# Performance work log

Measured on AMD Instinct MI355X. Metric: run time of the kernel, lower is better.

The kernel has to match this reference:

```python
import jax, jax.numpy as jnp
import numpy as np

B, S, H, D = 2, 2048, 16, 128
HID = H * D
THETA = 10000.0
SCALE = 1.0 / np.sqrt(D)


def setup_inputs() -> dict:
    key = jax.random.key(0)
    k1, k2, k3 = jax.random.split(key, 3)
    x = jax.random.normal(k1, (B, S, HID), dtype=jnp.float32)
    w_qkv = jax.random.normal(k2, (3 * HID, HID), dtype=jnp.float32) * 0.02
    w_o = jax.random.normal(k3, (HID, HID), dtype=jnp.float32) * 0.02
    return {"x": x, "w_qkv": w_qkv, "w_o": w_o}


def _rope_cos_sin(seq_len, dim, dtype):
    inv_freq = 1.0 / (THETA ** (jnp.arange(0, dim, 2, dtype=jnp.float32) / dim))
    pos = jnp.arange(seq_len, dtype=jnp.float32)
    freqs = pos[:, None] * inv_freq[None, :]          # (S, D/2)
    emb = jnp.concatenate([freqs, freqs], axis=-1)    # (S, D)
    return jnp.cos(emb).astype(dtype), jnp.sin(emb).astype(dtype)


def _rotate_half(t):
    t1, t2 = jnp.split(t, 2, axis=-1)
    return jnp.concatenate([-t2, t1], axis=-1)


def reference(x, w_qkv, w_o):
    b, s, _ = x.shape
    qkv = jnp.einsum('bsh,oh->bso', x, w_qkv)                 # (B,S,3*HID)
    qkv = qkv.reshape(b, s, 3, H, D).transpose(2, 0, 3, 1, 4)  # (3,B,H,S,D)
    q, k, v = qkv[0], qkv[1], qkv[2]
    cos, sin = _rope_cos_sin(s, D, x.dtype)                    # (S,D)
    q = q * cos + _rotate_half(q) * sin
    k = k * cos + _rotate_half(k) * sin
    scores = jnp.einsum('bhqd,bhkd->bhqk', q, k) * SCALE       # (B,H,S,S)
    causal = jnp.triu(jnp.ones((s, s), dtype=bool), k=1)
    scores = jnp.where(causal[None, None], -jnp.inf, scores)
    attn = jax.nn.softmax(scores.astype(jnp.float32), axis=-1).astype(q.dtype)
    out = jnp.einsum('bhqk,bhkd->bhqd', attn, v)               # (B,H,S,D)
    out = out.transpose(0, 2, 1, 3).reshape(b, s, HID)
    return jnp.einsum('bsh,oh->bso', out, w_o)
```

## Files before the change

### kernel.cpp

```cpp
#include <hip/hip_runtime.h>
#include <hip/hip_bf16.h>

typedef unsigned short u16;
typedef unsigned long long u64;
typedef u16 us8 __attribute__((ext_vector_type(8)));
typedef __bf16 bf8_t __attribute__((ext_vector_type(8)));
typedef float f32x4 __attribute__((ext_vector_type(4)));

__device__ __forceinline__ float b2f(u16 u) {
    return __uint_as_float(((unsigned int)u) << 16);
}
__device__ __forceinline__ u16 f2b(float f) {
    union { __hip_bfloat16 h; u16 u; } v;
    v.h = __float2bfloat16(f);
    return v.u;
}
__device__ __forceinline__ f32x4 mfma16(bf8_t a, bf8_t b, f32x4 c) {
    return __builtin_amdgcn_mfma_f32_16x16x32_bf16(a, b, c, 0, 0, 0);
}
__device__ __forceinline__ void gload_lds16(const u16* g, u16* lds_base) {
    __builtin_amdgcn_global_load_lds((const __attribute__((address_space(1))) unsigned int*)g,
                                     (__attribute__((address_space(3))) unsigned int*)lds_base,
                                     16, 0, 0);
}

__global__ __launch_bounds__(256) void f32_to_bf16(const float* __restrict__ src,
                                                   u16* __restrict__ dst, int n8) {
    int idx = blockIdx.x * 256 + threadIdx.x;
    if (idx >= n8) return;
    float4 f0 = ((const float4*)src)[idx * 2];
    float4 f1 = ((const float4*)src)[idx * 2 + 1];
    us8 o;
    o[0] = f2b(f0.x); o[1] = f2b(f0.y); o[2] = f2b(f0.z); o[3] = f2b(f0.w);
    o[4] = f2b(f1.x); o[5] = f2b(f1.y); o[6] = f2b(f1.z); o[7] = f2b(f1.w);
    ((us8*)dst)[idx] = o;
}

#define BARX() __builtin_amdgcn_s_barrier()
#define LGKM0() do { asm volatile("s_waitcnt lgkmcnt(0)" ::: "memory"); \
                     __builtin_amdgcn_sched_barrier(0); } while (0)
#define VM6()   do { asm volatile("s_waitcnt vmcnt(6)" ::: "memory"); \
                     __builtin_amdgcn_sched_barrier(0); } while (0)

template<int SF32>
__global__ __launch_bounds__(512, 2) void gemm256(const u16* __restrict__ A,
                                                  const u16* __restrict__ B,
                                                  void* __restrict__ Cout, int ldc) {
    __shared__ u16 LA[2][2][128 * 64];
    __shared__ u16 LB[2][128 * 64];

    const int tid = threadIdx.x;
    const int w = tid >> 6, lane = tid & 63;
    const int lm = lane & 15, lq = lane >> 4;
    const int wm = w >> 1, wn = w & 1;

    const int bid = blockIdx.x;
    const int nper = gridDim.x >> 3;
    const int wg = (bid & 7) * nper + (bid >> 3);
    const int mt = wg & 15, nt = wg >> 4;
    const int m0 = mt * 256, n0 = nt * 128;

    const int lp = lane ^ ((lane & 32) >> 4);
    const int srow = lp >> 3;
    const int scol = (lp & 7) * 8;

    const u16* Abase = A + (size_t)(m0 + srow) * 2048 + scol;
    const u16* Bbase = B + (size_t)(n0 + srow) * 2048 + scol;

#define STAGE_A(c, h, kt) do { \
    int _k0 = (kt) * 64; \
    _Pragma("unroll") \
    for (int i = 0; i < 2; i++) { \
        int R = w * 2 + i; \
        gload_lds16(Abase + (size_t)((h) * 128 + R * 8) * 2048 + _k0, &LA[c][h][R * 512]); \
    } } while (0)

#define STAGE_B(c, kt) do { \
    int _k0 = (kt) * 64; \
    _Pragma("unroll") \
    for (int i = 0; i < 2; i++) { \
        int R = w * 2 + i; \
        gload_lds16(Bbase + (size_t)(R * 8) * 2048 + _k0, &LB[c][R * 512]); \
    } } while (0)

    bf8_t af[4][2], bfr[4][2];
    f32x4 acc[4][4] = {};
    const int ahalf = wm >> 1;
    const int arbase = (wm & 1) * 64;
    const int brbase = wn * 64;

#define READ_FRAGS(c) do { \
    _Pragma("unroll") \
    for (int m = 0; m < 4; m++) { \
        int rl = arbase + m * 16 + lm; \
        _Pragma("unroll") \
        for (int ks = 0; ks < 2; ks++) { \
            int o = rl * 128 + ks * 64 + lq * 16; \
            o ^= ((o >> 9) & 1) << 5; \
            af[m][ks] = *(const bf8_t*)((const char*)&LA[c][ahalf][0] + o); \
        } \
    } \
    _Pragma("unroll") \
    for (int n = 0; n < 4; n++) { \
        int rl = brbase + n * 16 + lm; \
        _Pragma("unroll") \
        for (int ks = 0; ks < 2; ks++) { \
            int o = rl * 128 + ks * 64 + lq * 16; \
            o ^= ((o >> 9) & 1) << 5; \
            bfr[n][ks] = *(const bf8_t*)((const char*)&LB[c][0] + o); \
        } \
    } } while (0)

#define QUAD(mh, nh) do { \
    __builtin_amdgcn_s_setprio(1); \
    _Pragma("unroll") \
    for (int m = 0; m < 2; m++) \
    _Pragma("unroll") \
    for (int n = 0; n < 2; n++) \
    _Pragma("unroll") \
    for (int ks = 0; ks < 2; ks++) \
        acc[(mh)*2+m][(nh)*2+n] = \
            mfma16(af[(mh)*2+m][ks], bfr[(nh)*2+n][ks], acc[(mh)*2+m][(nh)*2+n]); \
    __builtin_amdgcn_s_setprio(0); \
    } while (0)

    STAGE_B(0, 0); STAGE_A(0, 0, 0); STAGE_A(0, 1, 0);
    STAGE_B(1, 1); STAGE_A(1, 0, 1); STAGE_A(1, 1, 1);
    VM6();
    BARX();

    for (int it = 0; it < 16; it++) {
        const int t2 = (2 * it + 2 < 32) ? 2 * it + 2 : 31;
        const int t3 = (2 * it + 3 < 32) ? 2 * it + 3 : 31;
        READ_FRAGS(0);
        BARX(); LGKM0();
        QUAD(0, 0);
        BARX();
        STAGE_B(0, t2);
        QUAD(0, 1);
        BARX();
        STAGE_A(0, 0, t2);
        QUAD(1, 0);
        BARX();
        STAGE_A(0, 1, t2);
        QUAD(1, 1);
        VM6();
        BARX();
        READ_FRAGS(1);
        BARX(); LGKM0();
        QUAD(0, 0);
        BARX();
        STAGE_B(1, t3);
        QUAD(0, 1);
        BARX();
        STAGE_A(1, 0, t3);
        QUAD(1, 0);
        BARX();
        STAGE_A(1, 1, t3);
        QUAD(1, 1);
        VM6();
        BARX();
    }

#pragma unroll
    for (int m = 0; m < 4; m++)
#pragma unroll
        for (int n = 0; n < 4; n++)
#pragma unroll
            for (int r = 0; r < 4; r++) {
                int row = m0 + wm * 64 + m * 16 + lq * 4 + r;
                int col = n0 + wn * 64 + n * 16 + lm;
                if (SF32)
                    ((float*)Cout)[(size_t)row * ldc + col] = acc[m][n][r];
                else
                    ((u16*)Cout)[(size_t)row * ldc + col] = f2b(acc[m][n][r]);
            }
}

__global__ __launch_bounds__(256) void rope_vt(u16* __restrict__ qkv, u16* __restrict__ VT) {
    __shared__ u16 T[64 * 136];
    const int tid = threadIdx.x;
    const int s0 = blockIdx.x * 64;
    const int bh = blockIdx.y;
    const int b = bh >> 4, h = bh & 15;
#pragma unroll
    for (int p = 0; p < 4; p++) {
        int sl = p * 16 + (tid >> 4);
        int d0 = (tid & 15) * 8;
        *(us8*)&T[sl * 136 + d0] =
            *(const us8*)(qkv + ((size_t)(b * 2048 + s0 + sl)) * 6144 + 4096 + h * 128 + d0);
    }
#pragma unroll
    for (int p = 0; p < 2; p++) {
        int task = p * 256 + tid;
        int sl = task >> 3;
        int jg = task & 7;
        size_t base = ((size_t)(b * 2048 + s0 + sl)) * 6144 + h * 128 + jg * 8;
        us8 qlo = *(const us8*)(qkv + base);
        us8 qhi = *(const us8*)(qkv + base + 64);
        us8 klo = *(const us8*)(qkv + base + 2048);
        us8 khi = *(const us8*)(qkv + base + 2048 + 64);
        us8 oql, oqh, okl, okh;
        float s = (float)(s0 + sl);
#pragma unroll
        for (int e = 0; e < 8; e++) {
            int j = jg * 8 + e;
            float inv = __expf((float)j * (-9.210340371976184f / 64.f));
            float ang = s * inv;
            float sn, c;
            __sincosf(ang, &sn, &c);
            float q1 = b2f(qlo[e]), q2 = b2f(qhi[e]);
            oql[e] = f2b(q1 * c - q2 * sn);
            oqh[e] = f2b(q2 * c + q1 * sn);
            float k1 = b2f(klo[e]), k2 = b2f(khi[e]);
            okl[e] = f2b(k1 * c - k2 * sn);
            okh[e] = f2b(k2 * c + k1 * sn);
        }
        *(us8*)(qkv + base) = oql;
        *(us8*)(qkv + base + 64) = oqh;
        *(us8*)(qkv + base + 2048) = okl;
        *(us8*)(qkv + base + 2048 + 64) = okh;
    }
    __syncthreads();
#pragma unroll
    for (int p = 0; p < 4; p++) {
        int idx = p * 256 + tid;
        int d = idx & 127;
        int sg = idx >> 7;
        us8 v;
#pragma unroll
        for (int i = 0; i < 8; i++) v[i] = T[(sg * 8 + i) * 136 + d];
        *(us8*)&VT[((size_t)bh * 128 + d) * 2048 + s0 + sg * 8] = v;
    }
}

#define ATT_SCALE 0.08838834764831845f

__global__ __launch_bounds__(256, 2) void attn_flash(const u16* __restrict__ qkv, const u16* __restrict__ VT,
                                                     u16* __restrict__ AO) {
    const int bid = blockIdx.x;
    const int swz = (bid & 7) * 64 + (bid >> 3);
    const int bh = swz >> 4;
    const int pair = swz & 15;
    const int b = bh >> 4, h = bh & 15;
    const int tid = threadIdx.x, lane = tid & 63, wave = tid >> 6;
    const int lm = lane & 15, lq = lane >> 4;

    const int jq0 = 31 - pair;
    const int jq1 = pair;
    const int ktmax = jq0;

    __shared__ u16 Kt[64 * 136];
    __shared__ u16 Vt[128 * 72];

    bf8_t qf[2][4];
#pragma unroll
    for (int qg = 0; qg < 2; qg++) {
        const int jqv = qg ? jq1 : jq0;
        const u16* Qrow = qkv + ((size_t)(b * 2048 + jqv * 64 + wave * 16 + lm)) * 6144 + h * 128;
#pragma unroll
        for (int ks = 0; ks < 4; ks++)
            qf[qg][ks] = *(const bf8_t*)(Qrow + ks * 32 + lq * 8);
    }

    f32x4 Of[2][8] = {};
    float mrun[2] = {-3.0e38f, -3.0e38f}, lrun[2] = {0.f, 0.f};

    const u16* Kbase = qkv + (size_t)b * 2048 * 6144 + 2048 + h * 128;
    const u16* VTbase = VT + (size_t)bh * 128 * 2048;

    const int krow = tid >> 4;
    const int kcol = (tid & 15) * 8;
    const int vrow = tid >> 3;
    const int vcol = (tid & 7) * 8;

    us8 kreg[4], vreg[4];
#pragma unroll
    for (int p = 0; p < 4; p++) {
        kreg[p] = *(const us8*)(Kbase + (size_t)(p * 16 + krow) * 6144 + kcol);
        vreg[p] = *(const us8*)(VTbase + (size_t)(p * 32 + vrow) * 2048 + vcol);
    }

    for (int kt = 0; kt <= ktmax; kt++) {
        __syncthreads();
#pragma unroll
        for (int p = 0; p < 4; p++) {
            *(us8*)&Kt[(p * 16 + krow) * 136 + kcol] = kreg[p];
            *(us8*)&Vt[(p * 32 + vrow) * 72 + vcol] = vreg[p];
        }
        __syncthreads();
        {
            int kn = (kt + 1 <= ktmax ? kt + 1 : ktmax) * 64;
#pragma unroll
            for (int p = 0; p < 4; p++) {
                kreg[p] = *(const us8*)(Kbase + (size_t)(kn + p * 16 + krow) * 6144 + kcol);
                vreg[p] = *(const us8*)(VTbase + (size_t)(p * 32 + vrow) * 2048 + kn + vcol);
            }
        }

        const bool act1 = (kt <= jq1);
        u64 pk[2][4];
#pragma unroll
        for (int qg = 0; qg < 2; qg++) {
            if (qg == 0 || act1) {
                const int jqv = qg ? jq1 : jq0;
                float sv[4][4];
#pragma unroll
                for (int nb = 0; nb < 4; nb++) {
                    f32x4 a = {};
#pragma unroll
                    for (int ks = 0; ks < 4; ks++) {
                        bf8_t kf = *(const bf8_t*)&Kt[(nb * 16 + lm) * 136 + ks * 32 + lq * 8];
                        a = mfma16(kf, qf[qg][ks], a);
                    }
#pragma unroll
                    for (int r = 0; r < 4; r++) sv[nb][r] = a[r] * ATT_SCALE;
                }
                if (kt == jqv) {
                    int qglob = jqv * 64 + wave * 16 + lm;
#pragma unroll
                    for (int nb = 0; nb < 4; nb++)
#pragma unroll
                        for (int r = 0; r < 4; r++)
                            if (kt * 64 + nb * 16 + lq * 4 + r > qglob) sv[nb][r] = -3.0e38f;
                }
                float mx = -3.0e38f;
#pragma unroll
                for (int nb = 0; nb < 4; nb++)
#pragma unroll
                    for (int r = 0; r < 4; r++) mx = fmaxf(mx, sv[nb][r]);
                mx = fmaxf(mx, __shfl_xor(mx, 16, 64));
                mx = fmaxf(mx, __shfl_xor(mx, 32, 64));
                float mnew = fmaxf(mrun[qg], mx);
                float a_ = __expf(mrun[qg] - mnew);
                float rs = 0.f;
#pragma unroll
                for (int nb = 0; nb < 4; nb++) {
                    float e0 = __expf(sv[nb][0] - mnew), e1 = __expf(sv[nb][1] - mnew);
                    float e2 = __expf(sv[nb][2] - mnew), e3 = __expf(sv[nb][3] - mnew);
                    rs += (e0 + e1) + (e2 + e3);
                    unsigned int lo = (unsigned int)f2b(e0) | ((unsigned int)f2b(e1) << 16);
                    unsigned int hi = (unsigned int)f2b(e2) | ((unsigned int)f2b(e3) << 16);
                    pk[qg][nb] = (u64)lo | ((u64)hi << 32);
                }
                rs += __shfl_xor(rs, 16, 64);
                rs += __shfl_xor(rs, 32, 64);
                lrun[qg] = lrun[qg] * a_ + rs;
                mrun[qg] = mnew;
#pragma unroll
                for (int db = 0; db < 8; db++)
#pragma unroll
                    for (int r = 0; r < 4; r++) Of[qg][db][r] *= a_;
            }
        }

        const int slo = ((lq & 1) * 2) * 16 + lm;
        const int shi = slo + 16;
        const bool sel = (lq >> 1) != 0;
#pragma unroll
        for (int kk = 0; kk < 2; kk++) {
            union { u64 v[2]; bf8_t f; } pf[2];
#pragma unroll
            for (int qg = 0; qg < 2; qg++) {
                if (qg == 0 || act1) {
                    u64 lo0 = __shfl(pk[qg][2 * kk + 0], slo, 64);
                    u64 lo1 = __shfl(pk[qg][2 * kk + 1], slo, 64);
                    u64 hi0 = __shfl(pk[qg][2 * kk + 0], shi, 64);
                    u64 hi1 = __shfl(pk[qg][2 * kk + 1], shi, 64);
                    pf[qg].v[0] = sel ? lo1 : lo0;
                    pf[qg].v[1] = sel ? hi1 : hi0;
                }
            }
#pragma unroll
            for (int db = 0; db < 8; db++) {
                bf8_t vf = *(const bf8_t*)&Vt[(db * 16 + lm) * 72 + kk * 32 + lq * 8];
                Of[0][db] = mfma16(vf, pf[0].f, Of[0][db]);
                if (act1) Of[1][db] = mfma16(vf, pf[1].f, Of[1][db]);
            }
        }
    }
#pragma unroll
    for (int qg = 0; qg < 2; qg++) {
        const int jqv = qg ? jq1 : jq0;
        float invl = 1.f / lrun[qg];
        size_t rowbase = (size_t)(b * 2048 + jqv * 64 + wave * 16 + lm) * 2048 + h * 128;
#pragma unroll
        for (int db = 0; db < 8; db++) {
            ushort4 o;
            o.x = f2b(Of[qg][db][0] * invl);
            o.y = f2b(Of[qg][db][1] * invl);
            o.z = f2b(Of[qg][db][2] * invl);
            o.w = f2b(Of[qg][db][3] * invl);
            *(ushort4*)(AO + rowbase + db * 16 + lq * 4) = o;
        }
    }
}

extern "C" void kernel_launch(void* const* d_in, const int* in_sizes, int n_in,
                              void* d_out, int out_size, void* d_ws, size_t ws_size,
                              hipStream_t stream) {
    const float* x     = (const float*)d_in[0];
    const float* w_qkv = (const float*)d_in[1];
    const float* w_o   = (const float*)d_in[2];
    float* out = (float*)d_out;
    u16* ws = (u16*)d_ws;

    u16* qkvb  = ws;
    u16* VT    = ws + 25165824;
    u16* AO    = ws + 33554432;
    u16* xb    = ws + 41943040;
    u16* wqkvb = ws + 50331648;
    u16* wob   = ws + 62914560;

    f32_to_bf16<<<4096, 256, 0, stream>>>(x, xb, 1048576);
    f32_to_bf16<<<6144, 256, 0, stream>>>(w_qkv, wqkvb, 1572864);
    f32_to_bf16<<<2048, 256, 0, stream>>>(w_o, wob, 524288);
    gemm256<0><<<768, 512, 0, stream>>>(xb, wqkvb, qkvb, 6144);
    rope_vt<<<dim3(32, 32), 256, 0, stream>>>(qkvb, VT);
    attn_flash<<<dim3(512), 256, 0, stream>>>(qkvb, VT, AO);
    gemm256<1><<<256, 512, 0, stream>>>(AO, wob, out, 2048);
}
```

Before: 403.5 us.

## Enlarge GEMM tile to 256x256 with staggered A/B double-buffer pipeline

The bf16 GEMM output tile grows from 256x128 to 256x256, with 8 waves arranged 2x4 so each wave owns 128x64 of the output, which halves the number of workgroups. The K-loop is rebuilt so B is prefetched into the other buffer and A into the current one at staggered points, with fragments read in halves between MFMA quads and a vmcnt(4) wait. The goal is better operand reuse per byte loaded and fewer blocks. In exchange LDS use doubles to 128KB and accumulator registers double, which likely limits occupancy to one block per CU, and the grid of 384 or 128 blocks may underfill a 256-CU device.

```diff
diff --git a/kernel.cpp b/kernel.cpp
--- a/kernel.cpp
+++ b/kernel.cpp
@@ -39,142 +39,143 @@
 #define BARX() __builtin_amdgcn_s_barrier()
 #define LGKM0() do { asm volatile("s_waitcnt lgkmcnt(0)" ::: "memory"); \
                      __builtin_amdgcn_sched_barrier(0); } while (0)
-#define VM6()   do { asm volatile("s_waitcnt vmcnt(6)" ::: "memory"); \
+#define VM4()   do { asm volatile("s_waitcnt vmcnt(4)" ::: "memory"); \
                      __builtin_amdgcn_sched_barrier(0); } while (0)
 
 template<int SF32>
 __global__ __launch_bounds__(512, 2) void gemm256(const u16* __restrict__ A,
                                                   const u16* __restrict__ B,
                                                   void* __restrict__ Cout, int ldc) {
-    __shared__ u16 LA[2][2][128 * 64];
-    __shared__ u16 LB[2][128 * 64];
+    __shared__ u16 LA[2][256 * 64];
+    __shared__ u16 LB[2][256 * 64];
 
     const int tid = threadIdx.x;
     const int w = tid >> 6, lane = tid & 63;
     const int lm = lane & 15, lq = lane >> 4;
-    const int wm = w >> 1, wn = w & 1;
+    const int wm = w >> 2, wn = w & 3;
 
     const int bid = blockIdx.x;
     const int nper = gridDim.x >> 3;
     const int wg = (bid & 7) * nper + (bid >> 3);
     const int mt = wg & 15, nt = wg >> 4;
-    const int m0 = mt * 256, n0 = nt * 128;
+    const int m0 = mt * 256, n0 = nt * 256;
 
     const int lp = lane ^ ((lane & 32) >> 4);
     const int srow = lp >> 3;
     const int scol = (lp & 7) * 8;
 
-    const u16* Abase = A + (size_t)(m0 + srow) * 2048 + scol;
-    const u16* Bbase = B + (size_t)(n0 + srow) * 2048 + scol;
+    const u16* Ag = A + (size_t)(m0 + srow) * 2048 + scol;
+    const u16* Bg = B + (size_t)(n0 + srow) * 2048 + scol;
 
 #define STAGE_A(c, h, kt) do { \
-    int _k0 = (kt) * 64; \
     _Pragma("unroll") \
     for (int i = 0; i < 2; i++) { \
         int R = w * 2 + i; \
-        gload_lds16(Abase + (size_t)((h) * 128 + R * 8) * 2048 + _k0, &LA[c][h][R * 512]); \
+        gload_lds16(Ag + (size_t)((h) * 128 + R * 8) * 2048 + (kt) * 64, \
+                    &LA[c][((h) * 128 + R * 8) * 64]); \
     } } while (0)
 
-#define STAGE_B(c, kt) do { \
-    int _k0 = (kt) * 64; \
+#define STAGE_B(c, h, kt) do { \
     _Pragma("unroll") \
     for (int i = 0; i < 2; i++) { \
         int R = w * 2 + i; \
-        gload_lds16(Bbase + (size_t)(R * 8) * 2048 + _k0, &LB[c][R * 512]); \
+        gload_lds16(Bg + (size_t)((h) * 128 + R * 8) * 2048 + (kt) * 64, \
+                    &LB[c][((h) * 128 + R * 8) * 64]); \
     } } while (0)
 
-    bf8_t af[4][2], bfr[4][2];
-    f32x4 acc[4][4] = {};
-    const int ahalf = wm >> 1;
-    const int arbase = (wm & 1) * 64;
-    const int brbase = wn * 64;
-
-#define READ_FRAGS(c) do { \
-    _Pragma("unroll") \
-    for (int m = 0; m < 4; m++) { \
-        int rl = arbase + m * 16 + lm; \
-        _Pragma("unroll") \
-        for (int ks = 0; ks < 2; ks++) { \
-            int o = rl * 128 + ks * 64 + lq * 16; \
-            o ^= ((o >> 9) & 1) << 5; \
-            af[m][ks] = *(const bf8_t*)((const char*)&LA[c][ahalf][0] + o); \
-        } \
-    } \
-    _Pragma("unroll") \
-    for (int n = 0; n < 4; n++) { \
-        int rl = brbase + n * 16 + lm; \
-        _Pragma("unroll") \
-        for (int ks = 0; ks < 2; ks++) { \
-            int o = rl * 128 + ks * 64 + lq * 16; \
-            o ^= ((o >> 9) & 1) << 5; \
-            bfr[n][ks] = *(const bf8_t*)((const char*)&LB[c][0] + o); \
-        } \
+    bf8_t af[8][2], bfr[4][2];
+    f32x4 acc[8][4] = {};
+
+#define RD_A(c, mh) do { \
+    _Pragma("unroll") \
+    for (int m = 0; m < 4; m++) \
+    _Pragma("unroll") \
+    for (int ks = 0; ks < 2; ks++) { \
+        int o = (wm * 128 + ((mh) * 4 + m) * 16 + lm) * 128 + ks * 64 + lq * 16; \
+        o ^= ((o >> 9) & 1) << 5; \
+        af[(mh) * 4 + m][ks] = *(const bf8_t*)((const char*)&LA[c][0] + o); \
+    } } while (0)
+
+#define RD_B(c, nh) do { \
+    _Pragma("unroll") \
+    for (int n = 0; n < 2; n++) \
+    _Pragma("unroll") \
+    for (int ks = 0; ks < 2; ks++) { \
+        int o = (wn * 64 + ((nh) * 2 + n) * 16 + lm) * 128 + ks * 64 + lq * 16; \
+        o ^= ((o >> 9) & 1) << 5; \
+        bfr[(nh) * 2 + n][ks] = *(const bf8_t*)((const char*)&LB[c][0] + o); \
     } } while (0)
 
 #define QUAD(mh, nh) do { \
     __builtin_amdgcn_s_setprio(1); \
     _Pragma("unroll") \
-    for (int m = 0; m < 2; m++) \
+    for (int m = 0; m < 4; m++) \
     _Pragma("unroll") \
     for (int n = 0; n < 2; n++) \
     _Pragma("unroll") \
     for (int ks = 0; ks < 2; ks++) \
-        acc[(mh)*2+m][(nh)*2+n] = \
-            mfma16(af[(mh)*2+m][ks], bfr[(nh)*2+n][ks], acc[(mh)*2+m][(nh)*2+n]); \
+        acc[(mh) * 4 + m][(nh) * 2 + n] = mfma16(af[(mh) * 4 + m][ks], \
+            bfr[(nh) * 2 + n][ks], acc[(mh) * 4 + m][(nh) * 2 + n]); \
     __builtin_amdgcn_s_setprio(0); \
     } while (0)
 
-    STAGE_B(0, 0); STAGE_A(0, 0, 0); STAGE_A(0, 1, 0);
-    STAGE_B(1, 1); STAGE_A(1, 0, 1); STAGE_A(1, 1, 1);
-    VM6();
+#define TILE(c, tB, tA) do { \
+    RD_A(c, 0); RD_B(c, 0); \
+    STAGE_B((c) ^ 1, 0, tB); \
+    BARX(); LGKM0(); \
+    QUAD(0, 0); \
+    BARX(); \
+    RD_A(c, 1); \
+    STAGE_B((c) ^ 1, 1, tB); \
+    BARX(); LGKM0(); \
+    QUAD(1, 0); \
+    BARX(); \
+    RD_B(c, 1); \
+    STAGE_A(c, 0, tA); \
+    BARX(); LGKM0(); \
+    QUAD(0, 1); \
+    BARX(); \
+    STAGE_A(c, 1, tA); \
+    QUAD(1, 1); \
+    VM4(); \
+    BARX(); \
+} while (0)
+
+    STAGE_A(0, 0, 0); STAGE_A(0, 1, 0);
+    STAGE_B(0, 0, 0); STAGE_B(0, 1, 0);
+    STAGE_A(1, 0, 1); STAGE_A(1, 1, 1);
+    VM4();
     BARX();
 
     for (int it = 0; it < 16; it++) {
-        const int t2 = (2 * it + 2 < 32) ? 2 * it + 2 : 31;
-        const int t3 = (2 * it + 3 < 32) ? 2 * it + 3 : 31;
-        READ_FRAGS(0);
-        BARX(); LGKM0();
-        QUAD(0, 0);
-        BARX();
-        STAGE_B(0, t2);
-        QUAD(0, 1);
-        BARX();
-        STAGE_A(0, 0, t2);
-        QUAD(1, 0);
-        BARX();
-        STAGE_A(0, 1, t2);
-        QUAD(1, 1);
-        VM6();
-        BARX();
-        READ_FRAGS(1);
-        BARX(); LGKM0();
-        QUAD(0, 0);
-        BARX();
-        STAGE_B(1, t3);
-        QUAD(0, 1);
-        BARX();
-        STAGE_A(1, 0, t3);
-        QUAD(1, 0);
-        BARX();
-        STAGE_A(1, 1, t3);
-        QUAD(1, 1);
-        VM6();
-        BARX();
-    }
-
-#pragma unroll
-    for (int m = 0; m < 4; m++)
+        const int t0 = 2 * it, t1 = 2 * it + 1;
+        const int tB0 = t1;
+        const int tA0 = (t0 + 2 < 32) ? t0 + 2 : 31;
+        const int tB1 = (t1 + 1 < 32) ? t1 + 1 : 31;
+        const int tA1 = (t1 + 2 < 32) ? t1 + 2 : 31;
+        TILE(0, tB0, tA0);
+        TILE(1, tB1, tA1);
+    }
+
+#pragma unroll
+    for (int m = 0; m < 8; m++)
 #pragma unroll
         for (int n = 0; n < 4; n++)
 #pragma unroll
             for (int r = 0; r < 4; r++) {
-                int row = m0 + wm * 64 + m * 16 + lq * 4 + r;
+                int row = m0 + wm * 128 + m * 16 + lq * 4 + r;
                 int col = n0 + wn * 64 + n * 16 + lm;
                 if (SF32)
                     ((float*)Cout)[(size_t)row * ldc + col] = acc[m][n][r];
                 else
                     ((u16*)Cout)[(size_t)row * ldc + col] = f2b(acc[m][n][r]);
             }
+#undef TILE
+#undef QUAD
+#undef RD_A
+#undef RD_B
+#undef STAGE_A
+#undef STAGE_B
 }
 
 __global__ __launch_bounds__(256) void rope_vt(u16* __restrict__ qkv, u16* __restrict__ VT) {
@@ -415,8 +416,8 @@
     f32_to_bf16<<<4096, 256, 0, stream>>>(x, xb, 1048576);
     f32_to_bf16<<<6144, 256, 0, stream>>>(w_qkv, wqkvb, 1572864);
     f32_to_bf16<<<2048, 256, 0, stream>>>(w_o, wob, 524288);
-    gemm256<0><<<768, 512, 0, stream>>>(xb, wqkvb, qkvb, 6144);
+    gemm256<0><<<384, 512, 0, stream>>>(xb, wqkvb, qkvb, 6144);
     rope_vt<<<dim3(32, 32), 256, 0, stream>>>(qkvb, VT);
     attn_flash<<<dim3(512), 256, 0, stream>>>(qkvb, VT, AO);
-    gemm256<1><<<256, 512, 0, stream>>>(AO, wob, out, 2048);
-}
+    gemm256<1><<<128, 512, 0, stream>>>(AO, wob, out, 2048);
+}
```

Result: slower. 454.2 us (+12.6%).
